# Optimization experiments

Hardware: AMD Instinct MI355X
Metric: run time of the kernel (lower is better)

Reference implementation:

```python
import jax, jax.numpy as jnp
import numpy as np
import math

B, S, D = 2, 2048, 512
H = 8
DEPTH = D // H
MAX_REL = 1024
NEG_INF = -1.0e9


def skew(t):
    # t: (..., r, c). Pad a zero column on the left, reshape to move relative
    # logits into their absolute positions (Music Transformer skew trick).
    r, c = t.shape[-2], t.shape[-1]
    padded = jnp.pad(t, [(0, 0)] * (t.ndim - 1) + [(1, 0)])
    s = padded.reshape(-1, c + 1, r)[:, 1:]
    return s.reshape(t.shape)


def setup_inputs() -> dict:
    key = jax.random.key(0)
    ks = jax.random.split(key, 12)
    sc = 1.0 / math.sqrt(D)
    return {
        "q": jax.random.normal(ks[0], (B, S, D), jnp.float32),
        "k": jax.random.normal(ks[1], (B, S, D), jnp.float32),
        "v": jax.random.normal(ks[2], (B, S, D), jnp.float32),
        "mask": jax.random.randint(ks[3], (B, 1, S, S), 0, 2, jnp.int32),
        "Wq_w": jax.random.normal(ks[4], (D, D), jnp.float32) * sc,
        "Wq_b": jnp.zeros((D,), jnp.float32),
        "Wk_w": jax.random.normal(ks[5], (D, D), jnp.float32) * sc,
        "Wk_b": jnp.zeros((D,), jnp.float32),
        "Wv_w": jax.random.normal(ks[6], (D, D), jnp.float32) * sc,
        "Wv_b": jnp.zeros((D,), jnp.float32),
        "E": jax.random.normal(ks[7], (MAX_REL, D), jnp.float32),
        "Wo_w": jax.random.normal(ks[8], (D, D), jnp.float32) * sc,
        "Wo_b": jnp.zeros((D,), jnp.float32),
    }


def reference(q, k, v, mask, Wq_w, Wq_b, Wk_w, Wk_b, Wv_w, Wv_b, E, Wo_w, Wo_b):
    # Linear projections (torch Linear: x @ W^T + b)
    qp = q @ Wq_w.T + Wq_b
    kp = k @ Wk_w.T + Wk_b
    vp = v @ Wv_w.T + Wv_b

    # Required relative position embeddings for seq_len S (S >= MAX_REL here:
    # repeat E[0] for the first S-MAX_REL positions, then the full table).
    n_rep = max(0, S - MAX_REL)
    e = jnp.concatenate([jnp.tile(E[0:1], (n_rep, 1)), E[max(0, MAX_REL - S):]], axis=0)  # (S, D)

    # Split heads: (B,S,D)->(B,H,S,depth); e: (S,D)->(H,S,depth)
    qh = qp.reshape(B, S, H, DEPTH).transpose(0, 2, 1, 3)
    kh = kp.reshape(B, S, H, DEPTH).transpose(0, 2, 1, 3)
    vh = vp.reshape(B, S, H, DEPTH).transpose(0, 2, 1, 3)
    eh = e.reshape(S, H, DEPTH).transpose(1, 0, 2)

    QKt = jnp.einsum('bhqd,bhkd->bhqk', qh, kh)
    Srel = skew(jnp.einsum('bhqd,hkd->bhqk', qh, eh))
    logits = (QKt + Srel) / math.sqrt(DEPTH)
    logits = logits + mask.astype(logits.dtype) * NEG_INF
    attn = jnp.einsum('bhqk,bhkd->bhqd', jax.nn.softmax(logits, axis=-1), vh)

    # Merge heads and output projection
    out = attn.transpose(0, 2, 1, 3).reshape(B, S, D)
    return out @ Wo_w.T + Wo_b
```

## Files before the change

kernel.cpp:

```cpp
#include <hip/hip_runtime.h>
#include <hip/hip_bf16.h>

#define BB 2
#define SS 2048
#define DD 512
#define HH 8
#define DP 64
#define MR 1024

typedef __attribute__((ext_vector_type(8))) short bf16x8;
typedef __attribute__((ext_vector_type(4))) float floatx4;

static __device__ __forceinline__ unsigned short f2b(float x) {
    __hip_bfloat16 h = __float2bfloat16(x);
    return *reinterpret_cast<unsigned short*>(&h);
}
static __device__ __forceinline__ float b2f(unsigned short u) {
    __hip_bfloat16 h = *reinterpret_cast<__hip_bfloat16*>(&u);
    return __bfloat162float(h);
}
static __device__ __forceinline__ void gll16(const void* g, void* l) {
    __builtin_amdgcn_global_load_lds(
        (const __attribute__((address_space(1))) void*)g,
        (__attribute__((address_space(3))) void*)l, 16, 0, 0);
}
static __device__ __forceinline__ int xoff(int ks, int quad, int row) {
    return (((ks * 4 + quad) ^ (row & 7)) * 16);
}

__global__ __launch_bounds__(256) void prep_kernel(
    const float* __restrict__ Wq, const float* __restrict__ Wk,
    const float* __restrict__ Wv, const float* __restrict__ Wo,
    const float* __restrict__ E,  const float* __restrict__ q,
    const float* __restrict__ k,  const float* __restrict__ v,
    const int* __restrict__ mask,
    unsigned short* __restrict__ Wqb, unsigned short* __restrict__ Wkb,
    unsigned short* __restrict__ Wvb, unsigned short* __restrict__ Wob,
    unsigned short* __restrict__ Eb,  unsigned short* __restrict__ qb16,
    unsigned short* __restrict__ kb16, unsigned short* __restrict__ vb16,
    unsigned long long* __restrict__ bits)
{
    const int blk = blockIdx.x;
    if (blk < 7680) {
        const int gid = blk * 256 + threadIdx.x;
        const float* src; unsigned short* dst; int off;
        if      (gid < 65536)   { src = Wq; dst = Wqb;  off = gid; }
        else if (gid < 131072)  { src = Wk; dst = Wkb;  off = gid - 65536; }
        else if (gid < 196608)  { src = Wv; dst = Wvb;  off = gid - 131072; }
        else if (gid < 262144)  { src = Wo; dst = Wob;  off = gid - 196608; }
        else if (gid < 393216)  { src = E;  dst = Eb;   off = gid - 262144; }
        else if (gid < 917504)  { src = q;  dst = qb16; off = gid - 393216; }
        else if (gid < 1441792) { src = k;  dst = kb16; off = gid - 917504; }
        else                    { src = v;  dst = vb16; off = gid - 1441792; }
        float4 x = ((const float4*)src)[off];
        ushort4 u; u.x = f2b(x.x); u.y = f2b(x.y); u.z = f2b(x.z); u.w = f2b(x.w);
        ((ushort4*)dst)[off] = u;
    } else {
        const size_t wid = (size_t)(blk - 7680) * 4 + (threadIdx.x >> 6);
        const int lane = threadIdx.x & 63;
        const int mv = mask[wid * 64 + lane];
        unsigned long long bal = __ballot(mv != 0);
        if (lane == 0) bits[wid] = bal;
    }
}

__global__ __launch_bounds__(256) void gemm_proj(
    const unsigned short* __restrict__ Xq, const unsigned short* __restrict__ Xk,
    const unsigned short* __restrict__ Xv,
    const unsigned short* __restrict__ Wqb, const unsigned short* __restrict__ Wkb,
    const unsigned short* __restrict__ Wvb,
    const float* __restrict__ bq, const float* __restrict__ bk,
    const float* __restrict__ bv,
    unsigned short* __restrict__ qp, unsigned short* __restrict__ kp,
    unsigned short* __restrict__ vpT)
{
    const int z = blockIdx.z;
    const unsigned short* A  = (z == 0) ? Xq : (z == 1) ? Xk : Xv;
    const unsigned short* Wb = (z == 0) ? Wqb : (z == 1) ? Wkb : Wvb;
    const float* bias        = (z == 0) ? bq : (z == 1) ? bk : bv;

    __shared__ __align__(16) char parena[12288];
    char* AsB = parena;
    char* WsB = parena + 4096;
    const int t = threadIdx.x, lane = t & 63, w = t >> 6;
    const int quad = lane >> 4, l15 = lane & 15;
    const int wm = w >> 1, wn = w & 1;
    const int m0 = blockIdx.x * 32, n0 = blockIdx.y * 64;

    const int pa = w * 64 + lane;
    const int arow = pa >> 3, acol = (pa & 7) ^ (arow & 7);
    int wrow[2], wcol[2];
#pragma unroll
    for (int i = 0; i < 2; i++) {
        const int c = w * 2 + i;
        const int p = c * 64 + lane;
        wrow[i] = p >> 3; wcol[i] = (p & 7) ^ (wrow[i] & 7);
    }

    floatx4 acc[2];
    acc[0] = (floatx4){0.f, 0.f, 0.f, 0.f};
    acc[1] = (floatx4){0.f, 0.f, 0.f, 0.f};

    for (int k0 = 0; k0 < 512; k0 += 64) {
        if (k0) __syncthreads();
        gll16(A + (size_t)(m0 + arow) * 512 + k0 + acol * 8, AsB + w * 1024);
#pragma unroll
        for (int i = 0; i < 2; i++)
            gll16(Wb + (size_t)(n0 + wrow[i]) * 512 + k0 + wcol[i] * 8,
                  WsB + (w * 2 + i) * 1024);
        __syncthreads();
#pragma unroll
        for (int ks = 0; ks < 2; ks++) {
            bf16x8 a0 = *(const bf16x8*)(AsB + (wm * 16 + l15) * 128 + xoff(ks, quad, l15));
            bf16x8 b0 = *(const bf16x8*)(WsB + (wn * 32 + l15) * 128 + xoff(ks, quad, l15));
            bf16x8 b1 = *(const bf16x8*)(WsB + (wn * 32 + 16 + l15) * 128 + xoff(ks, quad, l15));
            acc[0] = __builtin_amdgcn_mfma_f32_16x16x32_bf16(a0, b0, acc[0], 0, 0, 0);
            acc[1] = __builtin_amdgcn_mfma_f32_16x16x32_bf16(a0, b1, acc[1], 0, 0, 0);
        }
    }

    if (z < 2) {
        unsigned short* Out = (z == 0) ? qp : kp;
#pragma unroll
        for (int ct = 0; ct < 2; ct++) {
            const int n = n0 + wn * 32 + ct * 16 + l15;
            const float bvl = bias[n];
#pragma unroll
            for (int r = 0; r < 4; r++) {
                const size_t m = (size_t)(m0 + wm * 16 + quad * 4 + r);
                Out[m * 512 + n] = f2b(acc[ct][r] + bvl);
            }
        }
    } else {
        __syncthreads();
        unsigned short* Ls = (unsigned short*)parena;
#pragma unroll
        for (int ct = 0; ct < 2; ct++) {
            const int dcol = wn * 32 + ct * 16 + l15;
            const float bvl = bias[n0 + dcol];
#pragma unroll
            for (int r = 0; r < 4; r++) {
                const int srow = wm * 16 + quad * 4 + r;
                Ls[dcol * 40 + srow] = f2b(acc[ct][r] + bvl);
            }
        }
        __syncthreads();
        const int bb = blockIdx.x >> 6, s0 = (blockIdx.x & 63) * 32, hh = blockIdx.y;
        const int drow = t >> 2, sc8 = (t & 3) * 8;
        *(uint4*)&vpT[((size_t)(bb * 8 + hh) * 64 + drow) * SS + s0 + sc8] =
            *(const uint4*)&Ls[drow * 40 + sc8];
    }
}

__global__ __launch_bounds__(256) void gemm_out(
    const unsigned short* __restrict__ A, const unsigned short* __restrict__ Wb,
    const float* __restrict__ bias, float* __restrict__ Out)
{
    __shared__ __align__(16) char parena[12288];
    char* AsB = parena;
    char* WsB = parena + 4096;
    const int t = threadIdx.x, lane = t & 63, w = t >> 6;
    const int quad = lane >> 4, l15 = lane & 15;
    const int wm = w >> 1, wn = w & 1;
    const int m0 = blockIdx.x * 32, n0 = blockIdx.y * 64;

    const int pa = w * 64 + lane;
    const int arow = pa >> 3, acol = (pa & 7) ^ (arow & 7);
    int wrow[2], wcol[2];
#pragma unroll
    for (int i = 0; i < 2; i++) {
        const int c = w * 2 + i;
        const int p = c * 64 + lane;
        wrow[i] = p >> 3; wcol[i] = (p & 7) ^ (wrow[i] & 7);
    }

    floatx4 acc[2];
    acc[0] = (floatx4){0.f, 0.f, 0.f, 0.f};
    acc[1] = (floatx4){0.f, 0.f, 0.f, 0.f};

    for (int k0 = 0; k0 < 512; k0 += 64) {
        if (k0) __syncthreads();
        gll16(A + (size_t)(m0 + arow) * 512 + k0 + acol * 8, AsB + w * 1024);
#pragma unroll
        for (int i = 0; i < 2; i++)
            gll16(Wb + (size_t)(n0 + wrow[i]) * 512 + k0 + wcol[i] * 8,
                  WsB + (w * 2 + i) * 1024);
        __syncthreads();
#pragma unroll
        for (int ks = 0; ks < 2; ks++) {
            bf16x8 a0 = *(const bf16x8*)(AsB + (wm * 16 + l15) * 128 + xoff(ks, quad, l15));
            bf16x8 b0 = *(const bf16x8*)(WsB + (wn * 32 + l15) * 128 + xoff(ks, quad, l15));
            bf16x8 b1 = *(const bf16x8*)(WsB + (wn * 32 + 16 + l15) * 128 + xoff(ks, quad, l15));
            acc[0] = __builtin_amdgcn_mfma_f32_16x16x32_bf16(a0, b0, acc[0], 0, 0, 0);
            acc[1] = __builtin_amdgcn_mfma_f32_16x16x32_bf16(a0, b1, acc[1], 0, 0, 0);
        }
    }
#pragma unroll
    for (int ct = 0; ct < 2; ct++) {
        const int n = n0 + wn * 32 + ct * 16 + l15;
        const float bvl = bias[n];
#pragma unroll
        for (int r = 0; r < 4; r++) {
            const size_t m = (size_t)(m0 + wm * 16 + quad * 4 + r);
            Out[m * 512 + n] = acc[ct][r] + bvl;
        }
    }
}

__global__ __launch_bounds__(256) void relg_kernel(
    const unsigned short* __restrict__ qp, const unsigned short* __restrict__ Eb,
    unsigned short* __restrict__ G)
{
    __shared__ unsigned short Ls[64 * 72];
    const int t = threadIdx.x, lane = t & 63, w = t >> 6;
    const int quad = lane >> 4, l15 = lane & 15;
    const int bh = blockIdx.z, b = bh >> 3, h = bh & 7;
    const int i0b = blockIdx.x * 64, t0 = blockIdx.y * 64;

    const unsigned short* Ar = qp + ((size_t)b * SS + i0b + w * 16 + l15) * DD + h * DP;
    bf16x8 a0 = *(const bf16x8*)(Ar + quad * 8);
    bf16x8 a1 = *(const bf16x8*)(Ar + 32 + quad * 8);

    floatx4 acc[4];
#pragma unroll
    for (int ct = 0; ct < 4; ct++) acc[ct] = (floatx4){0.f, 0.f, 0.f, 0.f};
#pragma unroll
    for (int ct = 0; ct < 4; ct++) {
        const unsigned short* Br = Eb + (size_t)(t0 + ct * 16 + l15) * DD + h * DP;
        bf16x8 b0 = *(const bf16x8*)(Br + quad * 8);
        bf16x8 b1 = *(const bf16x8*)(Br + 32 + quad * 8);
        acc[ct] = __builtin_amdgcn_mfma_f32_16x16x32_bf16(a0, b0, acc[ct], 0, 0, 0);
        acc[ct] = __builtin_amdgcn_mfma_f32_16x16x32_bf16(a1, b1, acc[ct], 0, 0, 0);
    }
#pragma unroll
    for (int ct = 0; ct < 4; ct++)
#pragma unroll
        for (int r = 0; r < 4; r++)
            Ls[(w * 16 + quad * 4 + r) * 72 + ct * 16 + l15] = f2b(acc[ct][r]);
    __syncthreads();
#pragma unroll
    for (int p = 0; p < 2; p++) {
        const int idx = p * 256 + t;
        const int row = idx >> 3, c8 = (idx & 7) * 8;
        *(uint4*)&G[((size_t)bh * SS + i0b + row) * MR + t0 + c8] =
            *(const uint4*)&Ls[row * 72 + c8];
    }
}

struct RelPF { ushort4 hi; ushort4 lo; int path; };

static __device__ __forceinline__ void rel_issue(
    const unsigned short* __restrict__ pdiag, int i0w, int k0, int quad,
    RelPF pf[2])
{
#pragma unroll
    for (int ct = 0; ct < 2; ct++) {
        const int k0c = k0 + ct * 16;
        const int gj0 = k0c + quad * 4;
        const int dmax = i0w + 15 - k0c;
        const int dmin = i0w - (k0c + 15);
        int path;
        if (dmin >= MR) path = 0;
        else if (dmin >= 0 && dmax <= MR - 1) path = 1;
        else if (dmax <= -2 && dmin >= -(MR + 1)) path = 2;
        else if (dmax <= -(MR + 2)) path = 3;
        else path = 4;
        pf[ct].path = path;
        if (path == 1 || path == 4) {
            const unsigned short* p = pdiag + 1023 + gj0;
            pf[ct].hi.x = p[0]; pf[ct].hi.y = p[1];
            pf[ct].hi.z = p[2]; pf[ct].hi.w = p[3];
        }
        if (path == 3 || path == 4) {
            const unsigned short* p = pdiag + max(gj0 - 2, 0);
            pf[ct].lo.x = p[0]; pf[ct].lo.y = p[1];
            pf[ct].lo.z = p[2]; pf[ct].lo.w = p[3];
        }
    }
}

static __device__ __forceinline__ void rel_convert(
    const RelPF& pf, int gi, int k0c, int quad,
    float d0a, float d0b, float relc[4])
{
    const int path = pf.path;
    if (path == 0) {
        relc[0] = relc[1] = relc[2] = relc[3] = d0a;
    } else if (path == 1) {
        relc[0] = b2f(pf.hi.x); relc[1] = b2f(pf.hi.y);
        relc[2] = b2f(pf.hi.z); relc[3] = b2f(pf.hi.w);
    } else if (path == 2) {
        relc[0] = relc[1] = relc[2] = relc[3] = d0b;
    } else if (path == 3) {
        relc[0] = b2f(pf.lo.x); relc[1] = b2f(pf.lo.y);
        relc[2] = b2f(pf.lo.z); relc[3] = b2f(pf.lo.w);
    } else {
        const int gj0 = k0c + quad * 4;
        const unsigned short hv[4] = {pf.hi.x, pf.hi.y, pf.hi.z, pf.hi.w};
        const unsigned short lv[4] = {pf.lo.x, pf.lo.y, pf.lo.z, pf.lo.w};
#pragma unroll
        for (int r = 0; r < 4; r++) {
            const int dd = gi - (gj0 + r);
            float rl;
            if (dd >= MR) rl = d0a;
            else if (dd >= 0) rl = b2f(hv[r]);
            else if (dd == -1) rl = 0.0f;
            else if (dd >= -(MR + 1)) rl = d0b;
            else rl = b2f(lv[r]);
            relc[r] = rl;
        }
    }
}

__global__ __launch_bounds__(256, 4) void attn_kernel(
    const unsigned short* __restrict__ qp, const unsigned short* __restrict__ kp,
    const unsigned short* __restrict__ vpT, const unsigned int* __restrict__ mb32,
    const unsigned short* __restrict__ G, unsigned short* __restrict__ ao)
{
    __shared__ __align__(16) char smem[38016];
    const int t = threadIdx.x, lane = t & 63, w = t >> 6;
    const int quad = lane >> 4, l15 = lane & 15;
    const int wr = w >> 1, kh = w & 1;
    const int bh = blockIdx.y, b = bh >> 3, h = bh & 7;
    const int i0w = blockIdx.x * 32 + wr * 16;
    const int gi = i0w + l15;

    const unsigned short* kb = kp + (size_t)b * SS * DD + h * DP;
    const unsigned short* vb = vpT + (size_t)bh * DP * SS;
    const unsigned short* Gb = G + (size_t)bh * SS * MR;
    const unsigned int* mrow32 = mb32 + ((size_t)b * SS + gi) * 64;

    const unsigned short* qrow = qp + ((size_t)b * SS + gi) * DD + h * DP;
    bf16x8 qf0 = *(const bf16x8*)(qrow + quad * 8);
    bf16x8 qf1 = *(const bf16x8*)(qrow + 32 + quad * 8);

    const unsigned short* pdiag = Gb + (size_t)gi * 1023;
    const float d0a = b2f(Gb[(size_t)gi * MR]);
    const float d0b = b2f(Gb[(size_t)min(gi + 1, SS - 1) * MR]);

    char* Kh = smem + kh * 8192;
    char* Vh = smem + 16384 + kh * 8192;
    char* Pt = smem + 32768 + w * 1280;

    int kofs[2], vofs[2], dst[2];
#pragma unroll
    for (int i = 0; i < 2; i++) {
        const int c = wr * 2 + i;
        const int p = c * 64 + lane;
        const int krow = p >> 3, kcol = (p & 7) ^ (krow & 7);
        kofs[i] = krow * DD + kcol * 8;
        const int vrow = p >> 2, vcol = (p & 3) ^ (vrow & 3);
        vofs[i] = vrow * SS + vcol * 8;
        dst[i] = c * 1024;
    }

    floatx4 oacc[4];
#pragma unroll
    for (int ct = 0; ct < 4; ct++) oacc[ct] = (floatx4){0.f, 0.f, 0.f, 0.f};
    float lsum = 0.0f;

    {
        const int k0 = kh * 1024;
        gll16(kb + (size_t)k0 * DD + kofs[0], Kh + dst[0]);
        gll16(kb + (size_t)k0 * DD + kofs[1], Kh + dst[1]);
        gll16(vb + k0 + vofs[0], Vh + dst[0]);
        gll16(vb + k0 + vofs[1], Vh + dst[1]);
    }
    unsigned int mwv = mrow32[kh * 32];
    RelPF pf[2];
    rel_issue(pdiag, i0w, kh * 1024, quad, pf);

    for (int it = 0; it < 32; it++) {
        const int cur = it & 1;
        __syncthreads();
        if (it + 1 < 32) {
            const int k0n = kh * 1024 + (it + 1) * 32;
            const int nb = (cur ^ 1) * 4096;
            gll16(kb + (size_t)k0n * DD + kofs[0], Kh + nb + dst[0]);
            gll16(kb + (size_t)k0n * DD + kofs[1], Kh + nb + dst[1]);
            gll16(vb + k0n + vofs[0], Vh + nb + dst[0]);
            gll16(vb + k0n + vofs[1], Vh + nb + dst[1]);
        }
        const unsigned int mcur = mwv;

        float relc[2][4];
        rel_convert(pf[0], gi, kh * 1024 + it * 32,      quad, d0a, d0b, relc[0]);
        rel_convert(pf[1], gi, kh * 1024 + it * 32 + 16, quad, d0a, d0b, relc[1]);

        {
            const int itn = (it + 1 < 32) ? it + 1 : 31;
            mwv = mrow32[kh * 32 + itn];
            rel_issue(pdiag, i0w, kh * 1024 + itn * 32, quad, pf);
        }

        char* Kc = Kh + cur * 4096;
        char* Vc = Vh + cur * 4096;

        bf16x8 kf[2][2];
#pragma unroll
        for (int ct = 0; ct < 2; ct++) {
            const int row = ct * 16 + l15;
            kf[ct][0] = *(const bf16x8*)(Kc + row * 128 + ((quad ^ (l15 & 7)) * 16));
            kf[ct][1] = *(const bf16x8*)(Kc + row * 128 + (((4 + quad) ^ (l15 & 7)) * 16));
        }
        bf16x8 vf[4];
#pragma unroll
        for (int ct = 0; ct < 4; ct++) {
            const int drow = ct * 16 + l15;
            vf[ct] = *(const bf16x8*)(Vc + drow * 64 + ((quad ^ (drow & 3)) * 16));
        }

        floatx4 acc[2];
#pragma unroll
        for (int ct = 0; ct < 2; ct++) {
            const unsigned int nib = (mcur >> (ct * 16 + quad * 4)) & 0xFu;
            floatx4 a;
#pragma unroll
            for (int r = 0; r < 4; r++)
                a[r] = relc[ct][r] + (((nib >> r) & 1u) ? -8.0e9f : 0.0f);
            acc[ct] = a;
        }
        __builtin_amdgcn_s_setprio(1);
#pragma unroll
        for (int ct = 0; ct < 2; ct++) {
            acc[ct] = __builtin_amdgcn_mfma_f32_16x16x32_bf16(kf[ct][0], qf0, acc[ct], 0, 0, 0);
            acc[ct] = __builtin_amdgcn_mfma_f32_16x16x32_bf16(kf[ct][1], qf1, acc[ct], 0, 0, 0);
        }
        __builtin_amdgcn_s_setprio(0);

#pragma unroll
        for (int ct = 0; ct < 2; ct++) {
            const float p0 = __expf(acc[ct][0] * 0.125f - 18.75f);
            const float p1 = __expf(acc[ct][1] * 0.125f - 18.75f);
            const float p2 = __expf(acc[ct][2] * 0.125f - 18.75f);
            const float p3 = __expf(acc[ct][3] * 0.125f - 18.75f);
            lsum += (p0 + p1) + (p2 + p3);
            ushort4 u;
            u.x = f2b(p0); u.y = f2b(p1); u.z = f2b(p2); u.w = f2b(p3);
            *(ushort4*)(Pt + l15 * 80 + ct * 32 + quad * 8) = u;
        }

        bf16x8 pt = *(const bf16x8*)(Pt + l15 * 80 + quad * 16);
        __builtin_amdgcn_s_setprio(1);
#pragma unroll
        for (int ct = 0; ct < 4; ct++)
            oacc[ct] = __builtin_amdgcn_mfma_f32_16x16x32_bf16(vf[ct], pt, oacc[ct], 0, 0, 0);
        __builtin_amdgcn_s_setprio(0);
    }

    lsum += __shfl_xor(lsum, 16);
    lsum += __shfl_xor(lsum, 32);

    __syncthreads();
    float* OmW = (float*)(smem + wr * 4352);
    float* MlW = (float*)(smem + 37888);
    if (kh == 1) {
#pragma unroll
        for (int ct = 0; ct < 4; ct++)
            *(floatx4*)&OmW[l15 * 68 + ct * 16 + quad * 4] = oacc[ct];
        if (lane < 16) MlW[wr * 16 + lane] = lsum;
    }
    __syncthreads();
    if (kh == 0) {
        const float inv = 1.0f / (lsum + MlW[wr * 16 + l15]);
#pragma unroll
        for (int ct = 0; ct < 4; ct++) {
            floatx4 o1 = *(const floatx4*)&OmW[l15 * 68 + ct * 16 + quad * 4];
            ushort4 u;
            u.x = f2b((oacc[ct][0] + o1[0]) * inv);
            u.y = f2b((oacc[ct][1] + o1[1]) * inv);
            u.z = f2b((oacc[ct][2] + o1[2]) * inv);
            u.w = f2b((oacc[ct][3] + o1[3]) * inv);
            *(ushort4*)&ao[((size_t)b * SS + gi) * DD + h * DP + ct * 16 + quad * 4] = u;
        }
    }
}

extern "C" void kernel_launch(void* const* d_in, const int* in_sizes, int n_in,
                              void* d_out, int out_size, void* d_ws, size_t ws_size,
                              hipStream_t stream)
{
    const float* q    = (const float*)d_in[0];
    const float* k    = (const float*)d_in[1];
    const float* v    = (const float*)d_in[2];
    const int*   mask = (const int*)d_in[3];
    const float* Wq_w = (const float*)d_in[4];
    const float* Wq_b = (const float*)d_in[5];
    const float* Wk_w = (const float*)d_in[6];
    const float* Wk_b = (const float*)d_in[7];
    const float* Wv_w = (const float*)d_in[8];
    const float* Wv_b = (const float*)d_in[9];
    const float* E    = (const float*)d_in[10];
    const float* Wo_w = (const float*)d_in[11];
    const float* Wo_b = (const float*)d_in[12];
    float* out = (float*)d_out;

    char* ws = (char*)d_ws;
    unsigned short* G    = (unsigned short*)ws;
    unsigned short* qp   = (unsigned short*)(ws + 67108864);
    unsigned short* kp   = qp + 2097152;
    unsigned short* vpT  = kp + 2 * 2097152;
    unsigned short* qb16 = vpT + 2097152;
    unsigned short* kb16 = qb16 + 2097152;
    unsigned short* vb16 = kb16 + 2097152;
    unsigned short* aob  = qb16;
    unsigned long long* mbits = (unsigned long long*)(ws + 67108864 + 7 * 4194304);
    unsigned short* Wqb = (unsigned short*)(ws + 67108864 + 7 * 4194304 + 1048576);
    unsigned short* Wkb = Wqb + 262144;
    unsigned short* Wvb = Wkb + 262144;
    unsigned short* Wob = Wvb + 262144;
    unsigned short* Ebf = Wob + 262144;

    dim3 blk(256);
    hipLaunchKernelGGL(prep_kernel, dim3(40448), blk, 0, stream,
                       Wq_w, Wk_w, Wv_w, Wo_w, E, q, k, v, mask,
                       Wqb, Wkb, Wvb, Wob, Ebf, qb16, kb16, vb16, mbits);
    hipLaunchKernelGGL(gemm_proj, dim3(128, 8, 3), blk, 0, stream,
                       qb16, kb16, vb16, Wqb, Wkb, Wvb, Wq_b, Wk_b, Wv_b,
                       qp, kp, vpT);
    hipLaunchKernelGGL(relg_kernel, dim3(32, 16, 16), blk, 0, stream, qp, Ebf, G);
    hipLaunchKernelGGL(attn_kernel, dim3(64, 16), blk, 0, stream,
                       qp, kp, vpT, (const unsigned int*)mbits, G, aob);
    hipLaunchKernelGGL(gemm_out, dim3(128, 8), blk, 0, stream, aob, Wob, Wo_b, out);
}
```

Measured before the change: 253.7 us.

## Split attention keys four ways per block, load K/V directly, remap grid

Reworks the attention kernel so each block handles 16 query rows and its four wavefronts each cover a quarter of the keys, instead of two row groups with two key halves. K and V fragments are read straight from global memory into registers, replacing the LDS double-buffered global_load_lds staging and the per-iteration __syncthreads. The grid is flattened to 2048 blocks with an XCD-aware index remap, and the occupancy hint rises to 5. Shared memory drops, but each wave now does its own uncached-in-LDS K/V reads with no sharing across row groups, and the final merge reduces four partials instead of two.

```diff
diff --git a/kernel.cpp b/kernel.cpp
--- a/kernel.cpp
+++ b/kernel.cpp
@@ -312,17 +312,19 @@
     }
 }
 
-__global__ __launch_bounds__(256, 4) void attn_kernel(
+__global__ __launch_bounds__(256, 5) void attn_kernel(
     const unsigned short* __restrict__ qp, const unsigned short* __restrict__ kp,
     const unsigned short* __restrict__ vpT, const unsigned int* __restrict__ mb32,
     const unsigned short* __restrict__ G, unsigned short* __restrict__ ao)
 {
-    __shared__ __align__(16) char smem[38016];
-    const int t = threadIdx.x, lane = t & 63, w = t >> 6;
+    __shared__ __align__(16) char smem[18368];
+    const int t = threadIdx.x, lane = t & 63, khq = t >> 6;
     const int quad = lane >> 4, l15 = lane & 15;
-    const int wr = w >> 1, kh = w & 1;
-    const int bh = blockIdx.y, b = bh >> 3, h = bh & 7;
-    const int i0w = blockIdx.x * 32 + wr * 16;
+    const int wg = blockIdx.x;
+    const int idx = (wg & 7) * 256 + (wg >> 3);
+    const int bh = idx >> 7, qblk = idx & 127;
+    const int b = bh >> 3, h = bh & 7;
+    const int i0w = qblk * 16;
     const int gi = i0w + l15;
 
     const unsigned short* kb = kp + (size_t)b * SS * DD + h * DP;
@@ -338,76 +340,42 @@
     const float d0a = b2f(Gb[(size_t)gi * MR]);
     const float d0b = b2f(Gb[(size_t)min(gi + 1, SS - 1) * MR]);
 
-    char* Kh = smem + kh * 8192;
-    char* Vh = smem + 16384 + kh * 8192;
-    char* Pt = smem + 32768 + w * 1280;
-
-    int kofs[2], vofs[2], dst[2];
-#pragma unroll
-    for (int i = 0; i < 2; i++) {
-        const int c = wr * 2 + i;
-        const int p = c * 64 + lane;
-        const int krow = p >> 3, kcol = (p & 7) ^ (krow & 7);
-        kofs[i] = krow * DD + kcol * 8;
-        const int vrow = p >> 2, vcol = (p & 3) ^ (vrow & 3);
-        vofs[i] = vrow * SS + vcol * 8;
-        dst[i] = c * 1024;
-    }
+    char* Pt = smem + 13248 + khq * 1280;
 
     floatx4 oacc[4];
 #pragma unroll
     for (int ct = 0; ct < 4; ct++) oacc[ct] = (floatx4){0.f, 0.f, 0.f, 0.f};
     float lsum = 0.0f;
 
-    {
-        const int k0 = kh * 1024;
-        gll16(kb + (size_t)k0 * DD + kofs[0], Kh + dst[0]);
-        gll16(kb + (size_t)k0 * DD + kofs[1], Kh + dst[1]);
-        gll16(vb + k0 + vofs[0], Vh + dst[0]);
-        gll16(vb + k0 + vofs[1], Vh + dst[1]);
-    }
-    unsigned int mwv = mrow32[kh * 32];
+    unsigned int mwv = mrow32[khq * 16];
     RelPF pf[2];
-    rel_issue(pdiag, i0w, kh * 1024, quad, pf);
-
-    for (int it = 0; it < 32; it++) {
-        const int cur = it & 1;
-        __syncthreads();
-        if (it + 1 < 32) {
-            const int k0n = kh * 1024 + (it + 1) * 32;
-            const int nb = (cur ^ 1) * 4096;
-            gll16(kb + (size_t)k0n * DD + kofs[0], Kh + nb + dst[0]);
-            gll16(kb + (size_t)k0n * DD + kofs[1], Kh + nb + dst[1]);
-            gll16(vb + k0n + vofs[0], Vh + nb + dst[0]);
-            gll16(vb + k0n + vofs[1], Vh + nb + dst[1]);
-        }
+    rel_issue(pdiag, i0w, khq * 512, quad, pf);
+
+    for (int it = 0; it < 16; it++) {
+        const int k0 = khq * 512 + it * 32;
+
+        bf16x8 kf[2][2];
+#pragma unroll
+        for (int ct = 0; ct < 2; ct++) {
+            const unsigned short* kr = kb + (size_t)(k0 + ct * 16 + l15) * DD;
+            kf[ct][0] = *(const bf16x8*)(kr + quad * 8);
+            kf[ct][1] = *(const bf16x8*)(kr + 32 + quad * 8);
+        }
+        bf16x8 vf[4];
+#pragma unroll
+        for (int ct = 0; ct < 4; ct++)
+            vf[ct] = *(const bf16x8*)(vb + (size_t)(ct * 16 + l15) * SS + k0 + quad * 8);
+
         const unsigned int mcur = mwv;
 
         float relc[2][4];
-        rel_convert(pf[0], gi, kh * 1024 + it * 32,      quad, d0a, d0b, relc[0]);
-        rel_convert(pf[1], gi, kh * 1024 + it * 32 + 16, quad, d0a, d0b, relc[1]);
+        rel_convert(pf[0], gi, k0,      quad, d0a, d0b, relc[0]);
+        rel_convert(pf[1], gi, k0 + 16, quad, d0a, d0b, relc[1]);
 
         {
-            const int itn = (it + 1 < 32) ? it + 1 : 31;
-            mwv = mrow32[kh * 32 + itn];
-            rel_issue(pdiag, i0w, kh * 1024 + itn * 32, quad, pf);
-        }
-
-        char* Kc = Kh + cur * 4096;
-        char* Vc = Vh + cur * 4096;
-
-        bf16x8 kf[2][2];
-#pragma unroll
-        for (int ct = 0; ct < 2; ct++) {
-            const int row = ct * 16 + l15;
-            kf[ct][0] = *(const bf16x8*)(Kc + row * 128 + ((quad ^ (l15 & 7)) * 16));
-            kf[ct][1] = *(const bf16x8*)(Kc + row * 128 + (((4 + quad) ^ (l15 & 7)) * 16));
-        }
-        bf16x8 vf[4];
-#pragma unroll
-        for (int ct = 0; ct < 4; ct++) {
-            const int drow = ct * 16 + l15;
-            vf[ct] = *(const bf16x8*)(Vc + drow * 64 + ((quad ^ (drow & 3)) * 16));
+            const int itn = (it + 1 < 16) ? it + 1 : 15;
+            mwv = mrow32[khq * 16 + itn];
+            rel_issue(pdiag, i0w, khq * 512 + itn * 32, quad, pf);
         }
 
         floatx4 acc[2];
@@ -451,26 +419,32 @@
     lsum += __shfl_xor(lsum, 16);
     lsum += __shfl_xor(lsum, 32);
 
+    float* OmW = (float*)smem;
+    float* MlW = (float*)(smem + 13056);
+    if (khq > 0) {
+        float* Om = OmW + (size_t)(khq - 1) * 1088;
+#pragma unroll
+        for (int ct = 0; ct < 4; ct++)
+            *(floatx4*)&Om[l15 * 68 + ct * 16 + quad * 4] = oacc[ct];
+        if (lane < 16) MlW[(khq - 1) * 16 + lane] = lsum;
+    }
     __syncthreads();
-    float* OmW = (float*)(smem + wr * 4352);
-    float* MlW = (float*)(smem + 37888);
-    if (kh == 1) {
-#pragma unroll
-        for (int ct = 0; ct < 4; ct++)
-            *(floatx4*)&OmW[l15 * 68 + ct * 16 + quad * 4] = oacc[ct];
-        if (lane < 16) MlW[wr * 16 + lane] = lsum;
-    }
-    __syncthreads();
-    if (kh == 0) {
-        const float inv = 1.0f / (lsum + MlW[wr * 16 + l15]);
+    if (khq == 0) {
+        const float inv = 1.0f /
+            (lsum + MlW[l15] + MlW[16 + l15] + MlW[32 + l15]);
 #pragma unroll
         for (int ct = 0; ct < 4; ct++) {
-            floatx4 o1 = *(const floatx4*)&OmW[l15 * 68 + ct * 16 + quad * 4];
+            floatx4 o = oacc[ct];
+#pragma unroll
+            for (int s = 0; s < 3; s++) {
+                floatx4 o1 = *(const floatx4*)&OmW[(size_t)s * 1088 + l15 * 68 + ct * 16 + quad * 4];
+                o[0] += o1[0]; o[1] += o1[1]; o[2] += o1[2]; o[3] += o1[3];
+            }
             ushort4 u;
-            u.x = f2b((oacc[ct][0] + o1[0]) * inv);
-            u.y = f2b((oacc[ct][1] + o1[1]) * inv);
-            u.z = f2b((oacc[ct][2] + o1[2]) * inv);
-            u.w = f2b((oacc[ct][3] + o1[3]) * inv);
+            u.x = f2b(o[0] * inv);
+            u.y = f2b(o[1] * inv);
+            u.z = f2b(o[2] * inv);
+            u.w = f2b(o[3] * inv);
             *(ushort4*)&ao[((size_t)b * SS + gi) * DD + h * DP + ct * 16 + quad * 4] = u;
         }
     }
@@ -519,7 +493,7 @@
                        qb16, kb16, vb16, Wqb, Wkb, Wvb, Wq_b, Wk_b, Wv_b,
                        qp, kp, vpT);
     hipLaunchKernelGGL(relg_kernel, dim3(32, 16, 16), blk, 0, stream, qp, Ebf, G);
-    hipLaunchKernelGGL(attn_kernel, dim3(64, 16), blk, 0, stream,
+    hipLaunchKernelGGL(attn_kernel, dim3(2048), blk, 0, stream,
                        qp, kp, vpT, (const unsigned int*)mbits, G, aob);
     hipLaunchKernelGGL(gemm_out, dim3(128, 8), blk, 0, stream, aob, Wob, Wo_b, out);
 }
```

Result: slower. 381.6 us (+50.4%).

## Replace LDS P transpose with in-register permlane/swizzle shuffle and rotate key tiles

Applied to the files above, without the earlier changes.

Moves the softmax-probability tile from the C layout to the B-operand layout of the PV MFMA using v_permlane32_swap and ds_swizzle instead of a write and read through LDS. This drops the per-wave P scratch buffer and shrinks shared memory from 38016 to 32768 bytes, which may allow more resident blocks. It also rotates each block's starting key tile by blockIdx.x so that concurrent blocks spread their K/V/G reads, and computes exp as exp2 with a folded FMA. The risks are that the lane permutation could be wrong and that ds_swizzle still goes through the LDS crossbar.

```diff
diff --git a/kernel.cpp b/kernel.cpp
--- a/kernel.cpp
+++ b/kernel.cpp
@@ -18,6 +18,9 @@
 static __device__ __forceinline__ float b2f(unsigned short u) {
     __hip_bfloat16 h = *reinterpret_cast<__hip_bfloat16*>(&u);
     return __bfloat162float(h);
+}
+static __device__ __forceinline__ unsigned int pk2(float lo, float hi) {
+    return (unsigned int)f2b(lo) | ((unsigned int)f2b(hi) << 16);
 }
 static __device__ __forceinline__ void gll16(const void* g, void* l) {
     __builtin_amdgcn_global_load_lds(
@@ -317,13 +320,14 @@
     const unsigned short* __restrict__ vpT, const unsigned int* __restrict__ mb32,
     const unsigned short* __restrict__ G, unsigned short* __restrict__ ao)
 {
-    __shared__ __align__(16) char smem[38016];
+    __shared__ __align__(16) char smem[32768];
     const int t = threadIdx.x, lane = t & 63, w = t >> 6;
     const int quad = lane >> 4, l15 = lane & 15;
     const int wr = w >> 1, kh = w & 1;
     const int bh = blockIdx.y, b = bh >> 3, h = bh & 7;
     const int i0w = blockIdx.x * 32 + wr * 16;
     const int gi = i0w + l15;
+    const int rot = (blockIdx.x & 3) << 3;
 
     const unsigned short* kb = kp + (size_t)b * SS * DD + h * DP;
     const unsigned short* vb = vpT + (size_t)bh * DP * SS;
@@ -340,7 +344,6 @@
 
     char* Kh = smem + kh * 8192;
     char* Vh = smem + 16384 + kh * 8192;
-    char* Pt = smem + 32768 + w * 1280;
 
     int kofs[2], vofs[2], dst[2];
 #pragma unroll
@@ -360,21 +363,25 @@
     float lsum = 0.0f;
 
     {
-        const int k0 = kh * 1024;
+        const int k0 = kh * 1024 + rot * 32;
         gll16(kb + (size_t)k0 * DD + kofs[0], Kh + dst[0]);
         gll16(kb + (size_t)k0 * DD + kofs[1], Kh + dst[1]);
         gll16(vb + k0 + vofs[0], Vh + dst[0]);
         gll16(vb + k0 + vofs[1], Vh + dst[1]);
     }
-    unsigned int mwv = mrow32[kh * 32];
+    unsigned int mwv = mrow32[kh * 32 + rot];
     RelPF pf[2];
-    rel_issue(pdiag, i0w, kh * 1024, quad, pf);
+    rel_issue(pdiag, i0w, kh * 1024 + rot * 32, quad, pf);
+
+    const float C1 = 0.125f * 1.4426950408889634f;
+    const float C2 = -18.75f * 1.4426950408889634f;
 
     for (int it = 0; it < 32; it++) {
         const int cur = it & 1;
+        const int tlc = it ^ rot;
         __syncthreads();
         if (it + 1 < 32) {
-            const int k0n = kh * 1024 + (it + 1) * 32;
+            const int k0n = kh * 1024 + ((it + 1) ^ rot) * 32;
             const int nb = (cur ^ 1) * 4096;
             gll16(kb + (size_t)k0n * DD + kofs[0], Kh + nb + dst[0]);
             gll16(kb + (size_t)k0n * DD + kofs[1], Kh + nb + dst[1]);
@@ -384,13 +391,13 @@
         const unsigned int mcur = mwv;
 
         float relc[2][4];
-        rel_convert(pf[0], gi, kh * 1024 + it * 32,      quad, d0a, d0b, relc[0]);
-        rel_convert(pf[1], gi, kh * 1024 + it * 32 + 16, quad, d0a, d0b, relc[1]);
+        rel_convert(pf[0], gi, kh * 1024 + tlc * 32,      quad, d0a, d0b, relc[0]);
+        rel_convert(pf[1], gi, kh * 1024 + tlc * 32 + 16, quad, d0a, d0b, relc[1]);
 
         {
-            const int itn = (it + 1 < 32) ? it + 1 : 31;
-            mwv = mrow32[kh * 32 + itn];
-            rel_issue(pdiag, i0w, kh * 1024 + itn * 32, quad, pf);
+            const int tln = (it + 1 < 32) ? ((it + 1) ^ rot) : tlc;
+            mwv = mrow32[kh * 32 + tln];
+            rel_issue(pdiag, i0w, kh * 1024 + tln * 32, quad, pf);
         }
 
         char* Kc = Kh + cur * 4096;
@@ -428,19 +435,33 @@
         }
         __builtin_amdgcn_s_setprio(0);
 
+        float ps[2][4];
 #pragma unroll
         for (int ct = 0; ct < 2; ct++) {
-            const float p0 = __expf(acc[ct][0] * 0.125f - 18.75f);
-            const float p1 = __expf(acc[ct][1] * 0.125f - 18.75f);
-            const float p2 = __expf(acc[ct][2] * 0.125f - 18.75f);
-            const float p3 = __expf(acc[ct][3] * 0.125f - 18.75f);
-            lsum += (p0 + p1) + (p2 + p3);
-            ushort4 u;
-            u.x = f2b(p0); u.y = f2b(p1); u.z = f2b(p2); u.w = f2b(p3);
-            *(ushort4*)(Pt + l15 * 80 + ct * 32 + quad * 8) = u;
-        }
-
-        bf16x8 pt = *(const bf16x8*)(Pt + l15 * 80 + quad * 16);
+#pragma unroll
+            for (int r = 0; r < 4; r++)
+                ps[ct][r] = __builtin_exp2f(fmaf(acc[ct][r], C1, C2));
+            lsum += (ps[ct][0] + ps[ct][1]) + (ps[ct][2] + ps[ct][3]);
+        }
+
+        unsigned int s0 = pk2(ps[0][0], ps[0][1]);
+        unsigned int s1 = pk2(ps[1][0], ps[1][1]);
+        unsigned int s2 = pk2(ps[0][2], ps[0][3]);
+        unsigned int s3 = pk2(ps[1][2], ps[1][3]);
+        asm("v_permlane32_swap_b32 %0, %1" : "+v"(s0), "+v"(s1));
+        asm("v_permlane32_swap_b32 %0, %1" : "+v"(s2), "+v"(s3));
+        const unsigned int h0 = (unsigned int)__builtin_amdgcn_ds_swizzle((int)s0, 0x401F);
+        const unsigned int h1 = (unsigned int)__builtin_amdgcn_ds_swizzle((int)s1, 0x401F);
+        const unsigned int h2 = (unsigned int)__builtin_amdgcn_ds_swizzle((int)s2, 0x401F);
+        const unsigned int h3 = (unsigned int)__builtin_amdgcn_ds_swizzle((int)s3, 0x401F);
+        const bool ev = (quad & 1) == 0;
+        union { unsigned int wv[4]; bf16x8 v; } pu;
+        pu.wv[0] = ev ? s0 : h1;
+        pu.wv[1] = ev ? s2 : h3;
+        pu.wv[2] = ev ? h0 : s1;
+        pu.wv[3] = ev ? h2 : s3;
+        const bf16x8 pt = pu.v;
+
         __builtin_amdgcn_s_setprio(1);
 #pragma unroll
         for (int ct = 0; ct < 4; ct++)
@@ -453,7 +474,7 @@
 
     __syncthreads();
     float* OmW = (float*)(smem + wr * 4352);
-    float* MlW = (float*)(smem + 37888);
+    float* MlW = (float*)(smem + 8704);
     if (kh == 1) {
 #pragma unroll
         for (int ct = 0; ct < 4; ct++)
```

Measured after the change: 255.1 us. About the same (+0.5%).
